# Kernel tuning notes

Measured on AMD Instinct MI355X. Metric: run time of the kernel, lower is better.

Reference implementation:

```python
import jax, jax.numpy as jnp
import numpy as np

B, T, H, W, C = 2, 16, 56, 56, 128
K_T, K = 5, 7
HIDDEN = 4 * C  # expansion_ratio = 4


def kernel_to_freq_3d(kernel, t, h, w):
    # kernel: (C, k_t, k_h, k_w) -> (C, t, h, w) complex freq, centered circular placement
    c, k_t, k_h, k_w = kernel.shape
    t_idx = (jnp.arange(k_t) - k_t // 2) % t
    h_idx = (jnp.arange(k_h) - k_h // 2) % h
    w_idx = (jnp.arange(k_w) - k_w // 2) % w
    tt, th, tw = jnp.meshgrid(t_idx, h_idx, w_idx, indexing='ij')
    padded = jnp.zeros((c, t, h, w), kernel.dtype).at[:, tt, th, tw].set(kernel)
    return jnp.fft.fftn(padded, axes=(1, 2, 3))


def setup_inputs() -> dict:
    key = jax.random.key(0)
    ks = jax.random.split(key, 16)
    n = lambda k, shape, s=0.02: (jax.random.normal(k, shape, jnp.float32) * s)
    return {
        'x': jax.random.normal(ks[0], (B, T, H, W, C), jnp.float32),
        'Wg': n(ks[1], (C, C)), 'bg': jnp.zeros((C,), jnp.float32),
        'Wh': n(ks[2], (C, C)), 'bh': jnp.zeros((C,), jnp.float32),
        'gate_kernel': n(ks[3], (C, K_T, K, K), 0.05),
        'hidden_kernel': n(ks[4], (C, K_T, K, K), 0.05),
        'Wo': n(ks[5], (C, C)), 'bo': jnp.zeros((C,), jnp.float32),
        'ln_scale': jnp.ones((C,), jnp.float32), 'ln_bias': jnp.zeros((C,), jnp.float32),
        'W1': n(ks[6], (C, HIDDEN)), 'b1': jnp.zeros((HIDDEN,), jnp.float32),
        'W2': n(ks[7], (HIDDEN, C)), 'b2': jnp.zeros((C,), jnp.float32),
        'gamma': jnp.full((C,), 1e-6, jnp.float32),
    }


def reference(x, Wg, bg, Wh, bh, gate_kernel, hidden_kernel, Wo, bo,
              ln_scale, ln_bias, W1, b1, W2, b2, gamma):
    b, t, h, w, c = x.shape
    residual = x
    # --- GatedConvSSM3D ---
    gate_proj = x @ Wg + bg
    hidden_proj = x @ Wh + bh
    gk_f = kernel_to_freq_3d(gate_kernel, t, h, w).transpose(1, 2, 3, 0)   # (T,H,W,C)
    hk_f = kernel_to_freq_3d(hidden_kernel, t, h, w).transpose(1, 2, 3, 0)
    gate_spatial = jnp.fft.ifftn(jnp.fft.fftn(gate_proj, axes=(1, 2, 3)) * gk_f[None], axes=(1, 2, 3)).real
    hidden_spatial = jnp.fft.ifftn(jnp.fft.fftn(hidden_proj, axes=(1, 2, 3)) * hk_f[None], axes=(1, 2, 3)).real
    log_forget = -jax.nn.softplus(gate_spatial)          # log(1 - z)
    log_values = -jax.nn.softplus(-gate_spatial) + jnp.log(hidden_spatial ** 2 + 1e-6)  # log z + log h~

    def op(left, right):
        la, lb = left
        ra, rb = right
        return (la + ra, jnp.logaddexp(ra + lb, rb))

    # Heinsen scan along temporal axis (axis=1 of (B,T,H,W,C))
    _, log_h = jax.lax.associative_scan(op, (log_forget, log_values), axis=1)
    ssm_out = jnp.exp(log_h) @ Wo + bo
    # --- LayerNorm3D ---
    mean = jnp.mean(ssm_out, axis=-1, keepdims=True)
    var = jnp.var(ssm_out, axis=-1, keepdims=True)
    xn = (ssm_out - mean) / jnp.sqrt(var + 1e-6) * ln_scale + ln_bias
    # --- MLP + LayerScale + residual ---
    y = jax.nn.gelu(xn @ W1 + b1) @ W2 + b2
    return y * gamma + residual
```

## Files before the change

kernel.cpp:

```cpp
#include <hip/hip_runtime.h>
#include <hip/hip_bf16.h>
#include <hip/hip_fp16.h>
#include <cstdint>
#include <cstddef>

typedef unsigned short u16;
typedef __attribute__((ext_vector_type(8))) short bf16x8;
typedef __attribute__((ext_vector_type(4))) float f32x4;

#define MFMA16(a,b,c) __builtin_amdgcn_mfma_f32_16x16x32_bf16((a),(b),(c),0,0,0)


static __device__ __forceinline__ float b2f(u16 u){ return __uint_as_float(((unsigned)u)<<16); }
static __device__ __forceinline__ u16 f2b(float f){
  unsigned u = __float_as_uint(f);
  return (u16)((u + 0x7fffu + ((u>>16)&1u)) >> 16);
}
static __device__ __forceinline__ u16 f2h(float f){ return __half_as_ushort(__float2half(f)); }
static __device__ __forceinline__ __half2 u2h(unsigned u){ union{unsigned u;__half2 h;}c; c.u=u; return c.h; }

static __device__ __forceinline__ void gld_lds16(const void* g, void* l){
  __builtin_amdgcn_global_load_lds(
      (const __attribute__((address_space(1))) void*)g,
      (__attribute__((address_space(3))) void*)l, 16, 0, 0);
}

static __device__ __forceinline__ bool input_is_f32(const void* xp){
  const u16* u = (const u16*)xp;
  int cnt = 0;
#pragma unroll
  for (int i = 0; i < 64; ++i){
    unsigned e = (u[2*i] >> 7) & 0xFF;
    cnt += (e >= 100 && e <= 140) ? 1 : 0;
  }
  return cnt < 32;
}

static __device__ __forceinline__ u16 ldb(const void* p, int i, bool f32){
  return f32 ? f2b(((const float*)p)[i]) : ((const u16*)p)[i];
}
static __device__ __forceinline__ float ldf(const void* p, int i, bool f32){
  return f32 ? ((const float*)p)[i] : b2f(((const u16*)p)[i]);
}

__global__ __launch_bounds__(256) void k0_prep(
    const void* __restrict__ x,
    const void* __restrict__ Wg, const void* __restrict__ Wh, const void* __restrict__ Wo,
    const void* __restrict__ W1, const void* __restrict__ W2,
    const void* __restrict__ gk, const void* __restrict__ hk,
    const void* __restrict__ bg, const void* __restrict__ bh, const void* __restrict__ bo,
    const void* __restrict__ lns, const void* __restrict__ lnb,
    const void* __restrict__ b1, const void* __restrict__ b2, const void* __restrict__ gm,
    u16* __restrict__ XB,
    u16* __restrict__ WgT, u16* __restrict__ WhT, u16* __restrict__ WoT,
    u16* __restrict__ W1T, u16* __restrict__ W2T,
    unsigned* __restrict__ KWG, unsigned* __restrict__ KWH, u16* __restrict__ PRM)
{
  const bool f32 = input_is_f32(x);
  int tid = blockIdx.x*blockDim.x + threadIdx.x;
  int np  = gridDim.x*blockDim.x;

  if (f32){
    const float* xf = (const float*)x;
    for (int p = tid; p < 6422528; p += np){
      unsigned v = (unsigned)f2b(xf[2*p]) | ((unsigned)f2b(xf[2*p+1]) << 16);
      ((unsigned*)XB)[p] = v;
    }
  } else {
    const unsigned* xu = (const unsigned*)x;
    for (int p = tid; p < 6422528; p += np) ((unsigned*)XB)[p] = xu[p];
  }

  for (int p = tid; p < 16384; p += np){
    int n = p>>7, k = p&127;
    WgT[p] = ldb(Wg, k*128+n, f32);
    WhT[p] = ldb(Wh, k*128+n, f32);
    WoT[p] = ldb(Wo, k*128+n, f32);
  }
  for (int p = tid; p < 65536; p += np){
    int n = p>>7, k = p&127;
    W1T[p] = ldb(W1, k*512+n, f32);
  }
  for (int p = tid; p < 65536; p += np){
    int n = p>>9, k = p&511;
    W2T[p] = ldb(W2, k*128+n, f32);
  }
  for (int p = tid; p < 31360; p += np){
    int c = p / 245; int r = p - c*245;
    int j = r / 35;  int r2 = r - j*35;
    int k = r2 / 5;  int tap = r2 - k*5;
    int s = (c*5+tap)*49 + (j*7+k);
    unsigned g16 = f2h(ldf(gk, s, f32)), h16 = f2h(ldf(hk, s, f32));
    KWG[p] = g16 | (g16<<16);
    KWH[p] = h16 | (h16<<16);
  }
  for (int p = tid; p < 1408; p += np){
    const void* src; int off;
    if      (p < 128)  { src = bg;  off = p; }
    else if (p < 256)  { src = bh;  off = p-128; }
    else if (p < 384)  { src = bo;  off = p-256; }
    else if (p < 512)  { src = lns; off = p-384; }
    else if (p < 640)  { src = lnb; off = p-512; }
    else if (p < 1152) { src = b1;  off = p-640; }
    else if (p < 1280) { src = b2;  off = p-1152; }
    else               { src = gm;  off = p-1280; }
    PRM[p] = ldb(src, off, f32);
  }
}

__global__ __launch_bounds__(256) void k1_dualgemm(
    const u16* __restrict__ XB, const u16* __restrict__ WgT, const u16* __restrict__ WhT,
    const u16* __restrict__ PRM,
    u16* __restrict__ GP, u16* __restrict__ HP)
{
  int bid = blockIdx.x;
  int b = bid / 784; int hw = (bid % 784)*4 + (threadIdx.x >> 6);
  int lane = threadIdx.x & 63;
  int lrow = lane & 15, q = lane >> 4;

  bf16x8 a[4];
  const u16* xr = XB + ((size_t)(b*16 + lrow)*3136 + hw)*128 + q*8;
#pragma unroll
  for (int kt = 0; kt < 4; ++kt) a[kt] = *(const bf16x8*)(xr + kt*32);

#pragma unroll
  for (int mat = 0; mat < 2; ++mat){
    const u16* WT  = mat ? WhT : WgT;
    const u16* bia = PRM + (mat ? 128 : 0);
    u16* out       = mat ? HP  : GP;
#pragma unroll
    for (int nt = 0; nt < 8; ++nt){
      f32x4 acc = {0.f,0.f,0.f,0.f};
      const u16* wr = WT + (nt*16 + lrow)*128 + q*8;
#pragma unroll
      for (int kt = 0; kt < 4; ++kt){
        bf16x8 bfr = *(const bf16x8*)(wr + kt*32);
        acc = MFMA16(a[kt], bfr, acc);
      }
      int c = nt*16 + lrow;
      float bv = b2f(bia[c]);
      size_t base = (((size_t)(b*32 + (c>>2))*3136 + hw)*4 + (c&3))*16 + q*4;
      ushort4 pk;
      pk.x = f2h(acc[0] + bv); pk.y = f2h(acc[1] + bv);
      pk.z = f2h(acc[2] + bv); pk.w = f2h(acc[3] + bv);
      *(ushort4*)(out + base) = pk;
    }
  }
}

__global__ __launch_bounds__(256, 6) void k2_conv_scan(
    const u16* __restrict__ GP, const u16* __restrict__ HP,
    const unsigned* __restrict__ KWG, const unsigned* __restrict__ KWH,
    u16* __restrict__ ELH)
{
  __shared__ __align__(16) unsigned su[6272];

  int bid = blockIdx.x;
  int b = bid / 1568; int rr = bid - b*1568;
  int cg = rr / 49; int s = rr % 49;
  int th = s / 7, tw = s % 7;
  int tid = threadIdx.x;
  int h0g = th*8, w0g = tw*8;
  size_t tb = (size_t)(b*32 + cg)*200704;

  int wv = tid >> 6, lane = tid & 63;
  int cl = wv;
  int w0 = lane & 7, h0 = lane >> 3;

  int cu = __builtin_amdgcn_readfirstlane(cg*4 + wv);
  const unsigned* kwg = KWG + (size_t)cu*245;
  const unsigned* kwh = KWH + (size_t)cu*245;

  unsigned soff[4]; bool sval[4];
#pragma unroll
  for (int ss = 0; ss < 4; ++ss){
    int idx = wv*64 + ss*256 + lane;
    sval[ss] = (idx < 784);
    int pos = idx >> 2, d = idx & 3;
    int hh = pos / 14, ww = pos - hh*14;
    int pcl = d ^ (hh & 3);
    int hg = h0g + hh - 3; if (hg < 0) hg += 56; else if (hg >= 56) hg -= 56;
    int wg = w0g + ww - 3; if (wg < 0) wg += 56; else if (wg >= 56) wg -= 56;
    soff[ss] = (unsigned)(((hg*56 + wg)*4 + pcl)*32);
  }
  const char* gpb = (const char*)(GP + tb);
  const char* hpb = (const char*)(HP + tb);

  auto stagepass = [&](const char* Pb){
#pragma unroll
    for (int half = 0; half < 2; ++half){
#pragma unroll
      for (int ss = 0; ss < 4; ++ss){
        if (sval[ss])
          gld_lds16(Pb + soff[ss] + half*16,
                    (char*)su + half*12544 + (wv*64 + ss*256)*16);
      }
    }
  };
  auto convpass = [&](__half2* A, const unsigned* kw){
#pragma unroll
    for (int p = 0; p < 8; ++p) A[p] = u2h(0u);
    for (int j = 0; j < 7; ++j){
      int hh = h0 + 6 - j;
      int cb0 = (hh*14 + w0)*16 + ((cl ^ (hh & 3)) << 2);
      unsigned wj[35];
#pragma unroll
      for (int i = 0; i < 35; ++i) wj[i] = kw[j*35 + i];
#pragma unroll
      for (int k = 0; k < 7; ++k){
        const unsigned* sp = &su[cb0 + (6-k)*16];
        uint4 da = *(const uint4*)sp;
        uint4 db = *(const uint4*)(sp + 3136);
        unsigned P[8] = {da.x,da.y,da.z,da.w,db.x,db.y,db.z,db.w};
        unsigned M[8];
#pragma unroll
        for (int p = 0; p < 8; ++p) M[p] = (P[p]>>16) | (P[(p+1)&7]<<16);
#pragma unroll
        for (int p = 0; p < 8; ++p){
          A[p] = __hfma2(u2h(wj[k*5+0]), u2h(P[(p+1)&7]), A[p]);
          A[p] = __hfma2(u2h(wj[k*5+1]), u2h(M[p]),       A[p]);
          A[p] = __hfma2(u2h(wj[k*5+2]), u2h(P[p]),       A[p]);
          A[p] = __hfma2(u2h(wj[k*5+3]), u2h(M[(p+7)&7]), A[p]);
          A[p] = __hfma2(u2h(wj[k*5+4]), u2h(P[(p+7)&7]), A[p]);
        }
      }
    }
  };

  __half2 Ag[8], Ah[8];
  stagepass(gpb);
  __syncthreads();
  convpass(Ag, kwg);
  __syncthreads();
  stagepass(hpb);
  __syncthreads();
  convpass(Ah, kwh);

  float xg[16], xh[16];
#pragma unroll
  for (int p = 0; p < 8; ++p){
    float2 g2 = __half22float2(Ag[p]); xg[2*p] = g2.x; xg[2*p+1] = g2.y;
    float2 h2 = __half22float2(Ah[p]); xh[2*p] = h2.x; xh[2*p+1] = h2.y;
  }

  size_t ob = tb + ((size_t)(h0g + h0)*56 + (w0g + w0))*4 + cl;
  float lh = 0.f;
#pragma unroll
  for (int t = 0; t < 16; ++t){
    float g  = xg[t];
    float spg = fmaxf(g, 0.f) + __logf(1.f + __expf(-fabsf(g)));
    float lf  = -spg;
    float hv  = xh[t];
    float lv  = (g - spg) + __logf(hv*hv + 1e-6f);
    if (t == 0) lh = lv;
    else {
      float a_ = lf + lh;
      float mx = fmaxf(a_, lv);
      lh = mx + __logf(1.f + __expf(-fabsf(a_ - lv)));
    }
    ELH[ob + (size_t)t*12544] = f2b(__expf(lh));
  }
}

__global__ __launch_bounds__(256, 2) void k34_gemm_ln_mlp(
    const u16* __restrict__ ELH, const u16* __restrict__ WoT,
    const u16* __restrict__ W1T, const u16* __restrict__ W2T,
    const u16* __restrict__ PRM,
    const void* __restrict__ xraw, void* __restrict__ outv)
{
  __shared__ __align__(16) u16 smem[37376];
  u16* sW0 = smem;
  u16* sW1 = smem + 16384;
  u16* sXp = smem;
  u16* sH  = smem + 32768;

  int bid = blockIdx.x;
  int b = bid / 392; int rem = bid - b*392;
  int t2 = rem / 49; int s2 = rem - t2*49;
  int hw0 = s2 * 64;
  int tid = threadIdx.x;
  int wv = tid >> 6, lane = tid & 63;
  int lrow = lane & 15, q = lane >> 4;
  const bool f32io = input_is_f32(xraw);

  {
    int hw = hw0 + wv*16 + lrow;
    size_t tbA = ((size_t)(b*512) + t2)*3136;
    size_t tbB = tbA + (size_t)8*3136;
    union Cvt { uint4 u; bf16x8 v; };
    bf16x8 eA[4], eB[4];
#pragma unroll
    for (int kt = 0; kt < 4; ++kt){
      int cg0 = kt*8 + q*2;
      size_t eoA = (tbA + (size_t)cg0*50176 + hw)*4;
      size_t eoB = (tbB + (size_t)cg0*50176 + hw)*4;
      uint2 lo = *(const uint2*)(ELH + eoA);
      uint2 hi = *(const uint2*)(ELH + eoA + (size_t)50176*4);
      Cvt c1; c1.u = make_uint4(lo.x, lo.y, hi.x, hi.y); eA[kt] = c1.v;
      uint2 lo2 = *(const uint2*)(ELH + eoB);
      uint2 hi2 = *(const uint2*)(ELH + eoB + (size_t)50176*4);
      Cvt c2; c2.u = make_uint4(lo2.x, lo2.y, hi2.x, hi2.y); eB[kt] = c2.v;
    }

    float vA[8][4], vB[8][4];
#pragma unroll
    for (int nt = 0; nt < 8; ++nt){
      f32x4 aacc = {0.f,0.f,0.f,0.f}, bacc = {0.f,0.f,0.f,0.f};
      const u16* wr = WoT + (nt*16 + lrow)*128 + q*8;
#pragma unroll
      for (int kt = 0; kt < 4; ++kt){
        bf16x8 bfr = *(const bf16x8*)(wr + kt*32);
        aacc = MFMA16(eA[kt], bfr, aacc);
        bacc = MFMA16(eB[kt], bfr, bacc);
      }
      float bv = b2f(PRM[256 + nt*16 + lrow]);
#pragma unroll
      for (int i = 0; i < 4; ++i){ vA[nt][i] = aacc[i] + bv; vB[nt][i] = bacc[i] + bv; }
    }

#pragma unroll
    for (int i = 0; i < 4; ++i){
      float smA=0.f, sqA=0.f, smB=0.f, sqB=0.f;
#pragma unroll
      for (int nt = 0; nt < 8; ++nt){
        float a_ = vA[nt][i]; smA += a_; sqA = fmaf(a_, a_, sqA);
        float b_ = vB[nt][i]; smB += b_; sqB = fmaf(b_, b_, sqB);
      }
#pragma unroll
      for (int m = 1; m < 16; m <<= 1){
        smA += __shfl_xor(smA, m, 64); sqA += __shfl_xor(sqA, m, 64);
        smB += __shfl_xor(smB, m, 64); sqB += __shfl_xor(sqB, m, 64);
      }
      float mA = smA*(1.f/128.f), rA = rsqrtf(sqA*(1.f/128.f) - mA*mA + 1e-6f);
      float mB = smB*(1.f/128.f), rB = rsqrtf(sqB*(1.f/128.f) - mB*mB + 1e-6f);
      int r = wv*16 + q*4 + i;
#pragma unroll
      for (int nt = 0; nt < 8; ++nt){
        int c = nt*16 + lrow;
        float ls = b2f(PRM[384 + c]), lb = b2f(PRM[512 + c]);
        sXp[r*136 + c]        = f2b((vA[nt][i] - mA)*rA*ls + lb);
        sXp[8704 + r*136 + c] = f2b((vB[nt][i] - mB)*rB*ls + lb);
      }
    }
  }

  bf16x8 aA[4], aB[4];
#pragma unroll
  for (int kt = 0; kt < 4; ++kt){
    aA[kt] = *(const bf16x8*)&sXp[(wv*16 + lrow)*136 + kt*32 + q*8];
    aB[kt] = *(const bf16x8*)&sXp[8704 + (wv*16 + lrow)*136 + kt*32 + q*8];
  }
  __syncthreads();

  const u16* wsrc[8];
#pragma unroll
  for (int r = 0; r < 8; ++r){
    int c = r*4 + wv;
    if (c < 16){
      int j = c >> 2, kt = c & 3;
      wsrc[r] = W1T + (size_t)(j*16 + lrow)*128 + kt*32 + q*8;
    } else {
      int c2 = c - 16; int jo = c2 >> 1, kt2 = c2 & 1;
      wsrc[r] = W2T + (size_t)(jo*16 + lrow)*512 + kt2*32 + q*8;
    }
  }
  auto stage = [&](u16* buf, int nt){
#pragma unroll
    for (int r = 0; r < 8; ++r){
      int c = r*4 + wv;
      const u16* src = wsrc[r] + (c < 16 ? (size_t)nt*8192 : (size_t)nt*64);
      gld_lds16(src, buf + c*512);
    }
  };

  f32x4 accA[8], accB[8];
#pragma unroll
  for (int jo = 0; jo < 8; ++jo){ accA[jo] = (f32x4){0.f,0.f,0.f,0.f}; accB[jo] = (f32x4){0.f,0.f,0.f,0.f}; }
  u16* sHw = sH + wv*1152;

  stage(sW0, 0);
  asm volatile("s_waitcnt vmcnt(0)" ::: "memory");
  __builtin_amdgcn_s_barrier();

  auto mlpstep = [&](int nt, u16* wcur, u16* wnxt, bool do_stage){
    if (do_stage) stage(wnxt, nt+1);
#pragma unroll
    for (int js = 0; js < 4; ++js){
      f32x4 hc = {0.f,0.f,0.f,0.f};
#pragma unroll
      for (int kt = 0; kt < 4; ++kt)
        hc = MFMA16(aA[kt], *(const bf16x8*)&wcur[(js*4 + kt)*512 + lane*8], hc);
      float bv = b2f(PRM[640 + nt*64 + js*16 + lrow]);
#pragma unroll
      for (int i = 0; i < 4; ++i){
        float v = hc[i] + bv;
        float u = 0.79788456080286535588f*(v + 0.044715f*v*v*v);
        float su_ = __expf(-2.f*u);
        float gl = v * __builtin_amdgcn_rcpf(1.f + su_);
        sHw[(q*4 + i)*72 + js*16 + lrow] = (u16)(__float_as_uint(gl) >> 16);
      }
    }
#pragma unroll
    for (int kt2 = 0; kt2 < 2; ++kt2){
      bf16x8 af = *(const bf16x8*)&sHw[lrow*72 + kt2*32 + q*8];
#pragma unroll
      for (int jo = 0; jo < 8; ++jo)
        accA[jo] = MFMA16(af, *(const bf16x8*)&wcur[(16 + jo*2 + kt2)*512 + lane*8], accA[jo]);
    }
#pragma unroll
    for (int js = 0; js < 4; ++js){
      f32x4 hc = {0.f,0.f,0.f,0.f};
#pragma unroll
      for (int kt = 0; kt < 4; ++kt)
        hc = MFMA16(aB[kt], *(const bf16x8*)&wcur[(js*4 + kt)*512 + lane*8], hc);
      float bv = b2f(PRM[640 + nt*64 + js*16 + lrow]);
#pragma unroll
      for (int i = 0; i < 4; ++i){
        float v = hc[i] + bv;
        float u = 0.79788456080286535588f*(v + 0.044715f*v*v*v);
        float su_ = __expf(-2.f*u);
        float gl = v * __builtin_amdgcn_rcpf(1.f + su_);
        sHw[(q*4 + i)*72 + js*16 + lrow] = (u16)(__float_as_uint(gl) >> 16);
      }
    }
#pragma unroll
    for (int kt2 = 0; kt2 < 2; ++kt2){
      bf16x8 af = *(const bf16x8*)&sHw[lrow*72 + kt2*32 + q*8];
#pragma unroll
      for (int jo = 0; jo < 8; ++jo)
        accB[jo] = MFMA16(af, *(const bf16x8*)&wcur[(16 + jo*2 + kt2)*512 + lane*8], accB[jo]);
    }
    asm volatile("s_waitcnt vmcnt(0)" ::: "memory");
    __builtin_amdgcn_s_barrier();
  };

  for (int nt2 = 0; nt2 < 4; ++nt2){
    mlpstep(2*nt2,     sW0, sW1, true);
    mlpstep(2*nt2 + 1, sW1, sW0, nt2 < 3);
  }

  size_t rowA0 = ((size_t)(b*16 + t2))*3136 + hw0 + wv*16 + q*4;
  size_t rowB0 = rowA0 + (size_t)8*3136;
#pragma unroll
  for (int jo = 0; jo < 8; ++jo){
    int c = jo*16 + lrow;
    float bv  = b2f(PRM[1152 + c]);
    float gmv = b2f(PRM[1280 + c]);
#pragma unroll
    for (int i = 0; i < 4; ++i){
      size_t rA = rowA0 + i, rB = rowB0 + i;
      float yA = accA[jo][i] + bv, yB = accB[jo][i] + bv;
      if (f32io){
        float resA = ((const float*)xraw)[rA*128 + c];
        float resB = ((const float*)xraw)[rB*128 + c];
        ((float*)outv)[rA*128 + c] = yA*gmv + resA;
        ((float*)outv)[rB*128 + c] = yB*gmv + resB;
      } else {
        float resA = b2f(((const u16*)xraw)[rA*128 + c]);
        float resB = b2f(((const u16*)xraw)[rB*128 + c]);
        ((u16*)outv)[rA*128 + c] = f2b(yA*gmv + resA);
        ((u16*)outv)[rB*128 + c] = f2b(yB*gmv + resB);
      }
    }
  }
}

extern "C" void kernel_launch(void* const* d_in, const int* in_sizes, int n_in,
                              void* d_out, int out_size, void* d_ws, size_t ws_size,
                              hipStream_t stream)
{
  const void* x   = d_in[0];
  const void* Wg  = d_in[1];
  const void* bg  = d_in[2];
  const void* Wh  = d_in[3];
  const void* bh  = d_in[4];
  const void* gk  = d_in[5];
  const void* hk  = d_in[6];
  const void* Wo  = d_in[7];
  const void* bo  = d_in[8];
  const void* lns = d_in[9];
  const void* lnb = d_in[10];
  const void* W1  = d_in[11];
  const void* b1  = d_in[12];
  const void* W2  = d_in[13];
  const void* b2  = d_in[14];
  const void* gm  = d_in[15];

  char* ws = (char*)d_ws;
  u16* GP  = (u16*)(ws + 0);
  u16* HP  = (u16*)(ws + 25690112);
  u16* ELH = (u16*)(ws + 51380224);
  u16* XB  = (u16*)(ws + 77070336);
  u16* WgT = (u16*)(ws + 102760448);
  u16* WhT = WgT + 16384;
  u16* WoT = WhT + 16384;
  u16* W1T = WoT + 16384;
  u16* W2T = W1T + 65536;
  unsigned* KWG = (unsigned*)(W2T + 65536);
  unsigned* KWH = KWG + 50176;
  u16* PRM = (u16*)(KWH + 50176);

  k0_prep        <<<dim3(512),  dim3(256), 0, stream>>>(x, Wg, Wh, Wo, W1, W2, gk, hk,
                                                        bg, bh, bo, lns, lnb, b1, b2, gm,
                                                        XB, WgT, WhT, WoT, W1T, W2T, KWG, KWH, PRM);
  k1_dualgemm    <<<dim3(1568), dim3(256), 0, stream>>>(XB, WgT, WhT, PRM, GP, HP);
  k2_conv_scan   <<<dim3(3136), dim3(256), 0, stream>>>(GP, HP, KWG, KWH, ELH);
  k34_gemm_ln_mlp<<<dim3(784),  dim3(256), 0, stream>>>(ELH, WoT, W1T, W2T, PRM, x, (void*)d_out);
}
```

Baseline: 446.0 us.

## Recast depthwise 3D conv as MFMA with circulant temporal weight matrices

The depthwise 5x7x7 convolution in k2 moves off packed half2 FMAs and onto f16 MFMA instructions. The prep kernel now builds per-channel circulant (banded) temporal weight matrices for each spatial tap pair, and the conv kernel accumulates four 16x16 tiles per wave. The log-space Heinsen scan becomes a linear-space associative scan using warp shuffles across the 16 time rows, with sigmoid computed from the exponential. This trades a much larger weight buffer and less numerically robust linear-space products for far fewer vector ALU instructions in the conv stage.

New measurement: 398.5 us. 1.12x faster.

```diff
diff --git a/kernel.cpp b/kernel.cpp
--- a/kernel.cpp
+++ b/kernel.cpp
@@ -6,9 +6,11 @@
 
 typedef unsigned short u16;
 typedef __attribute__((ext_vector_type(8))) short bf16x8;
+typedef __attribute__((ext_vector_type(8))) _Float16 f16x8;
 typedef __attribute__((ext_vector_type(4))) float f32x4;
 
-#define MFMA16(a,b,c) __builtin_amdgcn_mfma_f32_16x16x32_bf16((a),(b),(c),0,0,0)
+#define MFMA16(a,b,c)  __builtin_amdgcn_mfma_f32_16x16x32_bf16((a),(b),(c),0,0,0)
+#define MFMAF16(a,b,c) __builtin_amdgcn_mfma_f32_16x16x32_f16((a),(b),(c),0,0,0)
 
 
 static __device__ __forceinline__ float b2f(u16 u){ return __uint_as_float(((unsigned)u)<<16); }
@@ -17,7 +19,8 @@
   return (u16)((u + 0x7fffu + ((u>>16)&1u)) >> 16);
 }
 static __device__ __forceinline__ u16 f2h(float f){ return __half_as_ushort(__float2half(f)); }
-static __device__ __forceinline__ __half2 u2h(unsigned u){ union{unsigned u;__half2 h;}c; c.u=u; return c.h; }
+
+union U4F { uint4 u; f16x8 h; };
 
 static __device__ __forceinline__ void gld_lds16(const void* g, void* l){
   __builtin_amdgcn_global_load_lds(
@@ -54,7 +57,7 @@
     u16* __restrict__ XB,
     u16* __restrict__ WgT, u16* __restrict__ WhT, u16* __restrict__ WoT,
     u16* __restrict__ W1T, u16* __restrict__ W2T,
-    unsigned* __restrict__ KWG, unsigned* __restrict__ KWH, u16* __restrict__ PRM)
+    unsigned* __restrict__ CIRG, unsigned* __restrict__ CIRH, u16* __restrict__ PRM)
 {
   const bool f32 = input_is_f32(x);
   int tid = blockIdx.x*blockDim.x + threadIdx.x;
@@ -85,15 +88,29 @@
     int n = p>>9, k = p&511;
     W2T[p] = ldb(W2, k*128+n, f32);
   }
-  for (int p = tid; p < 31360; p += np){
-    int c = p / 245; int r = p - c*245;
-    int j = r / 35;  int r2 = r - j*35;
-    int k = r2 / 5;  int tap = r2 - k*5;
-    int s = (c*5+tap)*49 + (j*7+k);
-    unsigned g16 = f2h(ldf(gk, s, f32)), h16 = f2h(ldf(hk, s, f32));
-    KWG[p] = g16 | (g16<<16);
-    KWH[p] = h16 | (h16<<16);
-  }
+
+  for (int p = tid; p < 819200; p += np){
+    int uu = p & 3;
+    int lane = (p >> 2) & 63;
+    int tpc = p >> 8;
+    int c = tpc / 25, tp = tpc - c*25;
+    int qq = lane >> 4, nn = lane & 15;
+    int tap = 2*tp + (qq >> 1);
+    unsigned vg = 0, vh = 0;
+    if (tap < 49){
+      int kk = ((qq & 1) << 3) + uu*2;
+      int i0 = (nn - kk + 2) & 15;
+      int i1 = (nn - kk + 1) & 15;
+      unsigned g0 = (i0 < 5) ? (unsigned)f2h(ldf(gk, c*245 + i0*49 + tap, f32)) : 0u;
+      unsigned h0 = (i0 < 5) ? (unsigned)f2h(ldf(hk, c*245 + i0*49 + tap, f32)) : 0u;
+      unsigned g1 = (i1 < 5) ? (unsigned)f2h(ldf(gk, c*245 + i1*49 + tap, f32)) : 0u;
+      unsigned h1 = (i1 < 5) ? (unsigned)f2h(ldf(hk, c*245 + i1*49 + tap, f32)) : 0u;
+      vg = g0 | (g1 << 16);
+      vh = h0 | (h1 << 16);
+    }
+    CIRG[p] = vg; CIRH[p] = vh;
+  }
+
   for (int p = tid; p < 1408; p += np){
     const void* src; int off;
     if      (p < 128)  { src = bg;  off = p; }
@@ -148,9 +165,9 @@
   }
 }
 
-__global__ __launch_bounds__(256, 6) void k2_conv_scan(
+__global__ __launch_bounds__(256, 5) void k2_conv_scan(
     const u16* __restrict__ GP, const u16* __restrict__ HP,
-    const unsigned* __restrict__ KWG, const unsigned* __restrict__ KWH,
+    const u16* __restrict__ CIRG, const u16* __restrict__ CIRH,
     u16* __restrict__ ELH)
 {
   __shared__ __align__(16) unsigned su[6272];
@@ -164,101 +181,110 @@
   size_t tb = (size_t)(b*32 + cg)*200704;
 
   int wv = tid >> 6, lane = tid & 63;
-  int cl = wv;
-  int w0 = lane & 7, h0 = lane >> 3;
+  int q = lane >> 4, lrow = lane & 15;
+  int hb = lrow >> 3, wb = lrow & 7;
 
   int cu = __builtin_amdgcn_readfirstlane(cg*4 + wv);
-  const unsigned* kwg = KWG + (size_t)cu*245;
-  const unsigned* kwh = KWH + (size_t)cu*245;
-
-  unsigned soff[4]; bool sval[4];
-#pragma unroll
-  for (int ss = 0; ss < 4; ++ss){
-    int idx = wv*64 + ss*256 + lane;
-    sval[ss] = (idx < 784);
-    int pos = idx >> 2, d = idx & 3;
+  const u16* cirg = CIRG + (size_t)cu*12800;
+  const u16* cirh = CIRH + (size_t)cu*12800;
+
+  unsigned soff[7]; bool sval[7];
+#pragma unroll
+  for (int ss = 0; ss < 7; ++ss){
+    int ci = ss*256 + tid;
+    sval[ss] = (ci < 1568);
+    int clc = ci / 392;
+    int rem = ci - clc*392;
+    int pos = rem >> 1, half = rem & 1;
     int hh = pos / 14, ww = pos - hh*14;
-    int pcl = d ^ (hh & 3);
     int hg = h0g + hh - 3; if (hg < 0) hg += 56; else if (hg >= 56) hg -= 56;
     int wg = w0g + ww - 3; if (wg < 0) wg += 56; else if (wg >= 56) wg -= 56;
-    soff[ss] = (unsigned)(((hg*56 + wg)*4 + pcl)*32);
+    soff[ss] = (unsigned)((hg*56 + wg)*128 + clc*32 + half*16);
   }
   const char* gpb = (const char*)(GP + tb);
   const char* hpb = (const char*)(HP + tb);
 
   auto stagepass = [&](const char* Pb){
 #pragma unroll
-    for (int half = 0; half < 2; ++half){
-#pragma unroll
-      for (int ss = 0; ss < 4; ++ss){
-        if (sval[ss])
-          gld_lds16(Pb + soff[ss] + half*16,
-                    (char*)su + half*12544 + (wv*64 + ss*256)*16);
-      }
+    for (int ss = 0; ss < 7; ++ss){
+      if (sval[ss])
+        gld_lds16(Pb + soff[ss], (char*)su + (ss*256 + wv*64)*16);
     }
   };
-  auto convpass = [&](__half2* A, const unsigned* kw){
-#pragma unroll
-    for (int p = 0; p < 8; ++p) A[p] = u2h(0u);
-    for (int j = 0; j < 7; ++j){
-      int hh = h0 + 6 - j;
-      int cb0 = (hh*14 + w0)*16 + ((cl ^ (hh & 3)) << 2);
-      unsigned wj[35];
-#pragma unroll
-      for (int i = 0; i < 35; ++i) wj[i] = kw[j*35 + i];
-#pragma unroll
-      for (int k = 0; k < 7; ++k){
-        const unsigned* sp = &su[cb0 + (6-k)*16];
-        uint4 da = *(const uint4*)sp;
-        uint4 db = *(const uint4*)(sp + 3136);
-        unsigned P[8] = {da.x,da.y,da.z,da.w,db.x,db.y,db.z,db.w};
-        unsigned M[8];
-#pragma unroll
-        for (int p = 0; p < 8; ++p) M[p] = (P[p]>>16) | (P[(p+1)&7]<<16);
-#pragma unroll
-        for (int p = 0; p < 8; ++p){
-          A[p] = __hfma2(u2h(wj[k*5+0]), u2h(P[(p+1)&7]), A[p]);
-          A[p] = __hfma2(u2h(wj[k*5+1]), u2h(M[p]),       A[p]);
-          A[p] = __hfma2(u2h(wj[k*5+2]), u2h(P[p]),       A[p]);
-          A[p] = __hfma2(u2h(wj[k*5+3]), u2h(M[(p+7)&7]), A[p]);
-          A[p] = __hfma2(u2h(wj[k*5+4]), u2h(P[(p+7)&7]), A[p]);
-        }
+
+  auto convpass = [&](const u16* cir, f32x4* acc){
+#pragma unroll
+    for (int m = 0; m < 4; ++m) acc[m] = (f32x4){0.f,0.f,0.f,0.f};
+    U4F bq0, bq1, bq2;
+    bq0.u = *(const uint4*)(cir + 0*512 + lane*8);
+    bq1.u = *(const uint4*)(cir + 1*512 + lane*8);
+    bq2.u = *(const uint4*)(cir + 2*512 + lane*8);
+    const int base_cl = wv*6272;
+#pragma unroll
+    for (int tp = 0; tp < 25; ++tp){
+      const int tA = 2*tp;
+      const int tB = (2*tp + 1 > 48) ? 48 : 2*tp + 1;
+      const int dhA = 6 - tA/7, dwA = 6 - tA%7;
+      const int dhB = 6 - tB/7, dwB = 6 - tB%7;
+      int dh = (q >= 2) ? dhB : dhA;
+      int dw = (q >= 2) ? dwB : dwA;
+      const char* sp = (const char*)su +
+          (base_cl + ((hb + dh)*14 + (wb + dw))*32 + (q & 1)*16);
+      U4F a0, a1, a2, a3;
+      a0.u = *(const uint4*)(sp);
+      a1.u = *(const uint4*)(sp + 896);
+      a2.u = *(const uint4*)(sp + 1792);
+      a3.u = *(const uint4*)(sp + 2688);
+      f16x8 bb = (tp % 3 == 0) ? bq0.h : (tp % 3 == 1) ? bq1.h : bq2.h;
+      acc[0] = MFMAF16(a0.h, bb, acc[0]);
+      acc[1] = MFMAF16(a1.h, bb, acc[1]);
+      acc[2] = MFMAF16(a2.h, bb, acc[2]);
+      acc[3] = MFMAF16(a3.h, bb, acc[3]);
+      if (tp + 3 < 25){
+        uint4 nb = *(const uint4*)(cir + (tp+3)*512 + lane*8);
+        if (tp % 3 == 0) bq0.u = nb; else if (tp % 3 == 1) bq1.u = nb; else bq2.u = nb;
       }
     }
   };
 
-  __half2 Ag[8], Ah[8];
+  f32x4 accG[4], accH[4];
   stagepass(gpb);
   __syncthreads();
-  convpass(Ag, kwg);
+  convpass(cirg, accG);
   __syncthreads();
   stagepass(hpb);
   __syncthreads();
-  convpass(Ah, kwh);
-
-  float xg[16], xh[16];
-#pragma unroll
-  for (int p = 0; p < 8; ++p){
-    float2 g2 = __half22float2(Ag[p]); xg[2*p] = g2.x; xg[2*p+1] = g2.y;
-    float2 h2 = __half22float2(Ah[p]); xh[2*p] = h2.x; xh[2*p+1] = h2.y;
-  }
-
-  size_t ob = tb + ((size_t)(h0g + h0)*56 + (w0g + w0))*4 + cl;
-  float lh = 0.f;
-#pragma unroll
-  for (int t = 0; t < 16; ++t){
-    float g  = xg[t];
-    float spg = fmaxf(g, 0.f) + __logf(1.f + __expf(-fabsf(g)));
-    float lf  = -spg;
-    float hv  = xh[t];
-    float lv  = (g - spg) + __logf(hv*hv + 1e-6f);
-    if (t == 0) lh = lv;
-    else {
-      float a_ = lf + lh;
-      float mx = fmaxf(a_, lv);
-      lh = mx + __logf(1.f + __expf(-fabsf(a_ - lv)));
-    }
-    ELH[ob + (size_t)t*12544] = f2b(__expf(lh));
+  convpass(cirh, accH);
+
+  float fv[16], vv[16];
+#pragma unroll
+  for (int e = 0; e < 16; ++e){
+    float g  = accG[e>>2][e&3];
+    float hc = accH[e>>2][e&3];
+    float eg = __expf(g);
+    float fr = __builtin_amdgcn_rcpf(1.f + eg);
+    float zz = 1.f - fr;
+    fv[e] = fr;
+    vv[e] = (hc*hc + 1e-6f) * zz;
+  }
+#pragma unroll
+  for (int d = 1; d < 16; d <<= 1){
+    bool ok = (lrow >= d);
+#pragma unroll
+    for (int e = 0; e < 16; ++e){
+      float Lf = __shfl_up(fv[e], (unsigned)d, 16);
+      float Lv = __shfl_up(vv[e], (unsigned)d, 16);
+      Lf = ok ? Lf : 1.f;
+      Lv = ok ? Lv : 0.f;
+      vv[e] = fmaf(fv[e], Lv, vv[e]);
+      fv[e] = fv[e] * Lf;
+    }
+  }
+  size_t ob = tb + (size_t)lrow*12544 + (size_t)(h0g*56 + w0g)*4 + wv;
+#pragma unroll
+  for (int e = 0; e < 16; ++e){
+    int r = (e>>2)*16 + q*4 + (e&3);
+    ELH[ob + (size_t)((r>>3)*56 + (r&7))*4] = f2b(vv[e]);
   }
 }
 
@@ -496,14 +522,14 @@
   u16* WoT = WhT + 16384;
   u16* W1T = WoT + 16384;
   u16* W2T = W1T + 65536;
-  unsigned* KWG = (unsigned*)(W2T + 65536);
-  unsigned* KWH = KWG + 50176;
-  u16* PRM = (u16*)(KWH + 50176);
+  unsigned* CIRG = (unsigned*)(W2T + 65536);
+  unsigned* CIRH = CIRG + 819200;
+  u16* PRM = (u16*)(CIRH + 819200);
 
   k0_prep        <<<dim3(512),  dim3(256), 0, stream>>>(x, Wg, Wh, Wo, W1, W2, gk, hk,
                                                         bg, bh, bo, lns, lnb, b1, b2, gm,
-                                                        XB, WgT, WhT, WoT, W1T, W2T, KWG, KWH, PRM);
+                                                        XB, WgT, WhT, WoT, W1T, W2T, CIRG, CIRH, PRM);
   k1_dualgemm    <<<dim3(1568), dim3(256), 0, stream>>>(XB, WgT, WhT, PRM, GP, HP);
-  k2_conv_scan   <<<dim3(3136), dim3(256), 0, stream>>>(GP, HP, KWG, KWH, ELH);
+  k2_conv_scan   <<<dim3(3136), dim3(256), 0, stream>>>(GP, HP, (const u16*)CIRG, (const u16*)CIRH, ELH);
   k34_gemm_ln_mlp<<<dim3(784),  dim3(256), 0, stream>>>(ELH, WoT, W1T, W2T, PRM, x, (void*)d_out);
 }
```
